# Optimization experiments

Measured on AMD Instinct MI355X. Metric: run time of the kernel, lower is better.

Reference implementation:

```python
import jax, jax.numpy as jnp
import numpy as np

B, C, HW = 32, 512, 4096
NUM_CLASSES = 80


def setup_inputs() -> dict:
    key = jax.random.key(0)
    k1, k2 = jax.random.split(key)
    feats = jax.random.normal(k1, (B, C, HW), dtype=jnp.float32)
    # Conv2d(feat_size, num_classes, 1, bias=False) weight -> [num_classes, feat_size]
    W = jax.random.normal(k2, (NUM_CLASSES, C), dtype=jnp.float32) * (1.0 / np.sqrt(C))
    return {"feats": feats, "W": W}


def reference(feats, W):
    # 1x1 conv == per-pixel matmul: [B,C,HW] x [N,C] -> [B,N,HW]
    att_logits = jnp.einsum('bch,nc->bnh', feats, W)
    att_maps = jax.nn.softmax(att_logits, axis=2)  # softmax over spatial dim HW
    # attention-weighted pooling: [B,N,HW] x [B,HW,C] -> [B,N,C]
    cls_feats = jnp.einsum('bnh,bch->bnc', att_maps, feats)
    return cls_feats
```

## Files before the change

kernel.cpp:

```cpp
#include <hip/hip_runtime.h>

#define B_ 32
#define C_ 512
#define HW_ 4096
#define N_ 80

typedef __bf16 bf16x8 __attribute__((ext_vector_type(8)));
typedef __bf16 bf16x4 __attribute__((ext_vector_type(4)));
typedef float f32x4 __attribute__((ext_vector_type(4)));
typedef unsigned short u16x8 __attribute__((ext_vector_type(8)));

__device__ __forceinline__ void gload_lds16(const void* g, void* l) {
  __builtin_amdgcn_global_load_lds((const __attribute__((address_space(1))) void*)g,
                                   (__attribute__((address_space(3))) void*)l, 16, 0, 0);
}

#define VMCNT(n) asm volatile("s_waitcnt vmcnt(" #n ")" ::: "memory")
#define SBAR() asm volatile("s_barrier" ::: "memory")

__global__ __launch_bounds__(256) void k0_wfrag(const float* __restrict__ W,
                                                __bf16* __restrict__ Wfrag,
                                                float* __restrict__ denom) {
  const int t = blockIdx.x * 256 + threadIdx.x;
  if (t < B_ * N_) denom[t] = 0.f;
  if (t >= 16 * 5 * 64) return;
  const int cs = t / 320, rem = t % 320;
  const int nf = rem >> 6, lane = rem & 63;
  const int n = nf * 16 + (lane & 15);
  const int c = cs * 32 + (lane >> 4) * 8;
  const float* wp = W + (size_t)n * C_ + c;
  bf16x8 v;
#pragma unroll
  for (int i = 0; i < 8; ++i) v[i] = (__bf16)wp[i];
  *(bf16x8*)(Wfrag + (size_t)t * 8) = v;
}

#define K1_STAGE(CS, SLOT)                                                      \
  {                                                                             \
    _Pragma("unroll") for (int j = 0; j < 4; ++j) {                             \
      const int d = j * 256 + tid;                                              \
      const int r = d >> 5, p = d & 31;                                         \
      gload_lds16(fb + (size_t)((CS)*32 + r) * HW_ + htile0 + p * 4,            \
                  (char*)tile + (SLOT)*16384 + (j * 256 + wave * 64) * 16);     \
    }                                                                           \
  }

#define K1_WLOAD(W, CS)                                                         \
  {                                                                             \
    _Pragma("unroll") for (int nf = 0; nf < 5; ++nf)                            \
        W[nf] = *(const u16x8*)(Wfrag + ((size_t)((CS)*5 + nf) * 64 + lane) * 8); \
  }

#define K1_COMPUTE(T, WU)                                                       \
  {                                                                             \
    const float* tb = (const float*)((char*)tile + ((T) % 3) * 16384);          \
    bf16x8 afr[2];                                                              \
    _Pragma("unroll") for (int hf = 0; hf < 2; ++hf) {                          \
      const int col = wave * 32 + hf * 16 + l16;                                \
      _Pragma("unroll") for (int i = 0; i < 8; ++i)                             \
          afr[hf][i] = (__bf16)tb[(quad * 8 + i) * 128 + col];                  \
    }                                                                           \
    _Pragma("unroll") for (int nf = 0; nf < 5; ++nf) {                          \
      const bf16x8 bfr = __builtin_bit_cast(bf16x8, WU[nf]);                    \
      acc[0][nf] = __builtin_amdgcn_mfma_f32_16x16x32_bf16(afr[0], bfr, acc[0][nf], 0, 0, 0); \
      acc[1][nf] = __builtin_amdgcn_mfma_f32_16x16x32_bf16(afr[1], bfr, acc[1][nf], 0, 0, 0); \
    }                                                                           \
  }

#define K1_ITER(T, WU, WL)                                                      \
  {                                                                             \
    VMCNT(9); SBAR();                                                           \
    K1_WLOAD(WL, (T) + 1);                                                      \
    if ((T) + 2 < 16) K1_STAGE((T) + 2, ((T) + 2) % 3);                         \
    K1_COMPUTE(T, WU);                                                          \
  }

__global__ __launch_bounds__(256, 3) void k1_logits(const float* __restrict__ feats,
                                                    const __bf16* __restrict__ Wfrag,
                                                    __bf16* __restrict__ E,
                                                    float* __restrict__ denom) {
  __shared__ float tile[3][32 * 128];
  const int tid = threadIdx.x;
  const int lane = tid & 63, wave = tid >> 6;
  const int quad = lane >> 4, l16 = lane & 15;
  const int b = blockIdx.y;
  const int htile0 = blockIdx.x * 128;
  const float* fb = feats + (size_t)b * (C_ * HW_);

  const f32x4 zero = {0.f, 0.f, 0.f, 0.f};
  f32x4 acc[2][5];
#pragma unroll
  for (int hf = 0; hf < 2; ++hf)
#pragma unroll
    for (int nf = 0; nf < 5; ++nf) acc[hf][nf] = zero;

  u16x8 wfA[5], wfB[5];
  K1_STAGE(0, 0);
  K1_WLOAD(wfA, 0);
  K1_STAGE(1, 1);

  for (int t = 0; t < 14; t += 2) {
    K1_ITER(t, wfA, wfB);
    K1_ITER(t + 1, wfB, wfA);
  }
  K1_ITER(14, wfA, wfB);
  VMCNT(5); SBAR();
  K1_COMPUTE(15, wfB);

#pragma unroll
  for (int nf = 0; nf < 5; ++nf) {
    const int n = nf * 16 + l16;
    float s = 0.f;
#pragma unroll
    for (int hf = 0; hf < 2; ++hf) {
      bf16x4 pk;
#pragma unroll
      for (int j = 0; j < 4; ++j) {
        const float e = __expf(acc[hf][nf][j]);
        s += e;
        pk[j] = (__bf16)e;
      }
      const int h = htile0 + wave * 32 + hf * 16 + quad * 4;
      *(bf16x4*)(E + (size_t)(b * N_ + n) * HW_ + h) = pk;
    }
    s += __shfl_xor(s, 16);
    s += __shfl_xor(s, 32);
    if (lane < 16) atomicAdd(denom + b * N_ + nf * 16 + lane, s);
  }
}

#define K3_STAGE(TK, SLOT)                                                      \
  {                                                                             \
    const int h0 = (TK)*64;                                                     \
    _Pragma("unroll") for (int j = 0; j < 2; ++j) {                             \
      const int d = j * 256 + tid;                                              \
      const int r = d >> 4, p = d & 15;                                         \
      gload_lds16(fb + (size_t)(c0 + r) * HW_ + h0 + ((p ^ (r & 15)) << 2),     \
                  (char*)fA + (SLOT)*8192 + (j * 256 + wave * 64) * 16);        \
    }                                                                           \
    _Pragma("unroll") for (int j = 0; j < 2; ++j) {                             \
      const int d = j * 256 + tid;                                              \
      const int r = d >> 3, p = d & 7;                                          \
      gload_lds16(eb + (size_t)r * HW_ + h0 + ((p ^ (r & 7)) << 3),             \
                  (char*)fB + (SLOT)*10240 + (j * 256 + wave * 64) * 16);       \
    }                                                                           \
    {                                                                           \
      const int d = 512 + (wave & 1) * 64 + lane;                               \
      const int r = d >> 3, p = d & 7;                                          \
      gload_lds16(eb + (size_t)r * HW_ + h0 + ((p ^ (r & 7)) << 3),             \
                  (char*)fB + (SLOT)*10240 + (512 + (wave & 1) * 64) * 16);     \
    }                                                                           \
  }

#define K3_COMPUTE(T)                                                           \
  {                                                                             \
    const float* A = (const float*)((char*)fA + ((T) % 4) * 8192);              \
    const __bf16* Bv = (const __bf16*)((char*)fB + ((T) % 4) * 10240);          \
    _Pragma("unroll") for (int ks = 0; ks < 2; ++ks) {                          \
      const int u0 = (ks * 8 + quad * 2) ^ l16;                                 \
      const int u1 = (ks * 8 + quad * 2 + 1) ^ l16;                             \
      const f32x4 va = *(const f32x4*)&A[rA * 64 + u0 * 4];                     \
      const f32x4 vb = *(const f32x4*)&A[rA * 64 + u1 * 4];                     \
      bf16x8 af;                                                                \
      af[0] = (__bf16)va[0]; af[1] = (__bf16)va[1];                             \
      af[2] = (__bf16)va[2]; af[3] = (__bf16)va[3];                             \
      af[4] = (__bf16)vb[0]; af[5] = (__bf16)vb[1];                             \
      af[6] = (__bf16)vb[2]; af[7] = (__bf16)vb[3];                             \
      _Pragma("unroll") for (int nfl = 0; nfl < 3; ++nfl) {                     \
        if (nfl >= nfcnt) break;                                                \
        const int n = (nfbase + nfl) * 16 + l16;                                \
        const int ub = (ks * 4 + quad) ^ (l16 & 7);                             \
        const u16x8 bv = *(const u16x8*)&Bv[n * 64 + ub * 8];                   \
        const bf16x8 bfr = __builtin_bit_cast(bf16x8, bv);                      \
        acc[nfl] = __builtin_amdgcn_mfma_f32_16x16x32_bf16(af, bfr, acc[nfl], 0, 0, 0); \
      }                                                                         \
    }                                                                           \
  }

__global__ __launch_bounds__(256, 2) void k3_pool(const float* __restrict__ feats,
                                                  const __bf16* __restrict__ E,
                                                  const float* __restrict__ denom,
                                                  float* __restrict__ out) {
  __shared__ float fA[4][32 * 64];
  __shared__ __bf16 fB[4][80 * 64];
  const int tid = threadIdx.x;
  const int lane = tid & 63, wave = tid >> 6;
  const int quad = lane >> 4, l16 = lane & 15;
  const int cf = wave & 1, ng = wave >> 1;
  const int nfbase = ng ? 3 : 0, nfcnt = ng ? 2 : 3;

  const int wg = blockIdx.x;
  const int nid = (wg & 7) * 64 + (wg >> 3);
  const int b = nid >> 4, cx = nid & 15;
  const int c0 = cx * 32;

  const float* fb = feats + (size_t)b * (C_ * HW_);
  const __bf16* eb = E + (size_t)b * N_ * HW_;
  const int rA = cf * 16 + l16;

  const f32x4 zero = {0.f, 0.f, 0.f, 0.f};
  f32x4 acc[3];
#pragma unroll
  for (int i = 0; i < 3; ++i) acc[i] = zero;

  K3_STAGE(0, 0);
  K3_STAGE(1, 1);
  K3_STAGE(2, 2);

  for (int t = 0; t < 61; ++t) {
    VMCNT(10); SBAR();
    K3_STAGE(t + 3, (t + 3) & 3);
    K3_COMPUTE(t);
  }
  VMCNT(10); SBAR(); K3_COMPUTE(61);
  VMCNT(5);  SBAR(); K3_COMPUTE(62);
  VMCNT(0);  SBAR(); K3_COMPUTE(63);

#pragma unroll
  for (int nfl = 0; nfl < 3; ++nfl) {
    if (nfl >= nfcnt) break;
    const int n = (nfbase + nfl) * 16 + l16;
    const float r = 1.0f / denom[b * N_ + n];
    float4 v;
    v.x = acc[nfl][0] * r; v.y = acc[nfl][1] * r;
    v.z = acc[nfl][2] * r; v.w = acc[nfl][3] * r;
    *(float4*)(out + (size_t)(b * N_ + n) * C_ + c0 + cf * 16 + quad * 4) = v;
  }
}

extern "C" void kernel_launch(void* const* d_in, const int* in_sizes, int n_in,
                              void* d_out, int out_size, void* d_ws, size_t ws_size,
                              hipStream_t stream) {
  (void)in_sizes; (void)n_in; (void)out_size; (void)ws_size;
  const float* feats = (const float*)d_in[0];
  const float* Wm = (const float*)d_in[1];
  float* out = (float*)d_out;

  __bf16* E = (__bf16*)d_ws;
  __bf16* Wfrag = E + (size_t)B_ * N_ * HW_;
  float* denom = (float*)(Wfrag + 16 * 5 * 64 * 8);

  hipLaunchKernelGGL(k0_wfrag, dim3(20), dim3(256), 0, stream, Wm, Wfrag, denom);
  hipLaunchKernelGGL(k1_logits, dim3(HW_ / 128, B_), dim3(256), 0, stream, feats, Wfrag, E, denom);
  hipLaunchKernelGGL(k3_pool, dim3(512), dim3(256), 0, stream, feats, E, denom, out);
}
```

Before: 122.3 us.

## Double k3_pool waves to 8 and halve the HW tile per stage

The pooling kernel now runs 512 threads (8 waves) per block instead of 256. The N dimension is split across 4 wave groups (2+1+1+1 fragments), and each pipeline stage covers a 32-wide HW tile instead of 64, which doubles the loop trip count and halves LDS use per stage. Only some lanes issue the global-to-LDS loads, and the wait counts are retuned. The goal is more waves per CU to hide memory latency and better MFMA balance. The cost is twice as many barriers, smaller transfers per stage, and an uneven split of work across waves.

```diff
diff --git a/kernel.cpp b/kernel.cpp
--- a/kernel.cpp
+++ b/kernel.cpp
@@ -131,63 +131,56 @@
 
 #define K3_STAGE(TK, SLOT)                                                      \
   {                                                                             \
-    const int h0 = (TK)*64;                                                     \
-    _Pragma("unroll") for (int j = 0; j < 2; ++j) {                             \
-      const int d = j * 256 + tid;                                              \
-      const int r = d >> 4, p = d & 15;                                         \
-      gload_lds16(fb + (size_t)(c0 + r) * HW_ + h0 + ((p ^ (r & 15)) << 2),     \
-                  (char*)fA + (SLOT)*8192 + (j * 256 + wave * 64) * 16);        \
-    }                                                                           \
-    _Pragma("unroll") for (int j = 0; j < 2; ++j) {                             \
-      const int d = j * 256 + tid;                                              \
+    const int h0 = (TK)*32;                                                     \
+    if (lane < 32) {                                                            \
+      const int d = wave * 32 + lane;                                           \
       const int r = d >> 3, p = d & 7;                                          \
-      gload_lds16(eb + (size_t)r * HW_ + h0 + ((p ^ (r & 7)) << 3),             \
-                  (char*)fB + (SLOT)*10240 + (j * 256 + wave * 64) * 16);       \
-    }                                                                           \
-    {                                                                           \
-      const int d = 512 + (wave & 1) * 64 + lane;                               \
-      const int r = d >> 3, p = d & 7;                                          \
-      gload_lds16(eb + (size_t)r * HW_ + h0 + ((p ^ (r & 7)) << 3),             \
-                  (char*)fB + (SLOT)*10240 + (512 + (wave & 1) * 64) * 16);     \
+      gload_lds16(fb + (size_t)(c0 + r) * HW_ + h0 + ((p ^ (r & 7)) << 2),      \
+                  (char*)fA + (SLOT)*4096 + wave * 512);                        \
+    }                                                                           \
+    if (lane < 40) {                                                            \
+      const int d = wave * 40 + lane;                                           \
+      const int r = d >> 2, p = d & 3;                                          \
+      gload_lds16(eb + (size_t)r * HW_ + h0 + ((p ^ (r & 3)) << 3),             \
+                  (char*)fB + (SLOT)*5120 + wave * 640);                        \
     }                                                                           \
   }
 
 #define K3_COMPUTE(T)                                                           \
   {                                                                             \
-    const float* A = (const float*)((char*)fA + ((T) % 4) * 8192);              \
-    const __bf16* Bv = (const __bf16*)((char*)fB + ((T) % 4) * 10240);          \
-    _Pragma("unroll") for (int ks = 0; ks < 2; ++ks) {                          \
-      const int u0 = (ks * 8 + quad * 2) ^ l16;                                 \
-      const int u1 = (ks * 8 + quad * 2 + 1) ^ l16;                             \
-      const f32x4 va = *(const f32x4*)&A[rA * 64 + u0 * 4];                     \
-      const f32x4 vb = *(const f32x4*)&A[rA * 64 + u1 * 4];                     \
-      bf16x8 af;                                                                \
-      af[0] = (__bf16)va[0]; af[1] = (__bf16)va[1];                             \
-      af[2] = (__bf16)va[2]; af[3] = (__bf16)va[3];                             \
-      af[4] = (__bf16)vb[0]; af[5] = (__bf16)vb[1];                             \
-      af[6] = (__bf16)vb[2]; af[7] = (__bf16)vb[3];                             \
-      _Pragma("unroll") for (int nfl = 0; nfl < 3; ++nfl) {                     \
-        if (nfl >= nfcnt) break;                                                \
-        const int n = (nfbase + nfl) * 16 + l16;                                \
-        const int ub = (ks * 4 + quad) ^ (l16 & 7);                             \
-        const u16x8 bv = *(const u16x8*)&Bv[n * 64 + ub * 8];                   \
-        const bf16x8 bfr = __builtin_bit_cast(bf16x8, bv);                      \
-        acc[nfl] = __builtin_amdgcn_mfma_f32_16x16x32_bf16(af, bfr, acc[nfl], 0, 0, 0); \
-      }                                                                         \
-    }                                                                           \
-  }
-
-__global__ __launch_bounds__(256, 2) void k3_pool(const float* __restrict__ feats,
+    const float* A = (const float*)((char*)fA + ((T) & 3) * 4096);              \
+    const __bf16* Bv = (const __bf16*)((char*)fB + ((T) & 3) * 5120);           \
+    const int u0 = (quad * 2) ^ (l16 & 7);                                      \
+    const int u1 = (quad * 2 + 1) ^ (l16 & 7);                                  \
+    const f32x4 va = *(const f32x4*)&A[rA * 32 + u0 * 4];                       \
+    const f32x4 vb = *(const f32x4*)&A[rA * 32 + u1 * 4];                       \
+    bf16x8 af;                                                                  \
+    af[0] = (__bf16)va[0]; af[1] = (__bf16)va[1];                               \
+    af[2] = (__bf16)va[2]; af[3] = (__bf16)va[3];                               \
+    af[4] = (__bf16)vb[0]; af[5] = (__bf16)vb[1];                               \
+    af[6] = (__bf16)vb[2]; af[7] = (__bf16)vb[3];                               \
+    _Pragma("unroll") for (int nfl = 0; nfl < 2; ++nfl) {                       \
+      if (nfl >= nfcnt) break;                                                  \
+      const int n = (nfbase + nfl) * 16 + l16;                                  \
+      const int ub = quad ^ (l16 & 3);                                          \
+      const u16x8 bv = *(const u16x8*)&Bv[n * 32 + ub * 8];                     \
+      const bf16x8 bfr = __builtin_bit_cast(bf16x8, bv);                        \
+      acc[nfl] = __builtin_amdgcn_mfma_f32_16x16x32_bf16(af, bfr, acc[nfl], 0, 0, 0); \
+    }                                                                           \
+  }
+
+__global__ __launch_bounds__(512, 2) void k3_pool(const float* __restrict__ feats,
                                                   const __bf16* __restrict__ E,
                                                   const float* __restrict__ denom,
                                                   float* __restrict__ out) {
-  __shared__ float fA[4][32 * 64];
-  __shared__ __bf16 fB[4][80 * 64];
+  __shared__ float fA[4 * 32 * 32];
+  __shared__ __bf16 fB[4 * 80 * 32];
   const int tid = threadIdx.x;
   const int lane = tid & 63, wave = tid >> 6;
   const int quad = lane >> 4, l16 = lane & 15;
   const int cf = wave & 1, ng = wave >> 1;
-  const int nfbase = ng ? 3 : 0, nfcnt = ng ? 2 : 3;
+  const int nfbase = (ng == 0) ? 0 : (ng + 1);
+  const int nfcnt = (ng == 0) ? 2 : 1;
 
   const int wg = blockIdx.x;
   const int nid = (wg & 7) * 64 + (wg >> 3);
@@ -197,27 +190,27 @@
   const float* fb = feats + (size_t)b * (C_ * HW_);
   const __bf16* eb = E + (size_t)b * N_ * HW_;
   const int rA = cf * 16 + l16;
-
   const f32x4 zero = {0.f, 0.f, 0.f, 0.f};
-  f32x4 acc[3];
-#pragma unroll
-  for (int i = 0; i < 3; ++i) acc[i] = zero;
+
+  f32x4 acc[2];
+  acc[0] = zero;
+  acc[1] = zero;
 
   K3_STAGE(0, 0);
   K3_STAGE(1, 1);
   K3_STAGE(2, 2);
 
-  for (int t = 0; t < 61; ++t) {
-    VMCNT(10); SBAR();
+  for (int t = 0; t < 125; ++t) {
+    VMCNT(4); SBAR();
     K3_STAGE(t + 3, (t + 3) & 3);
     K3_COMPUTE(t);
   }
-  VMCNT(10); SBAR(); K3_COMPUTE(61);
-  VMCNT(5);  SBAR(); K3_COMPUTE(62);
-  VMCNT(0);  SBAR(); K3_COMPUTE(63);
-
-#pragma unroll
-  for (int nfl = 0; nfl < 3; ++nfl) {
+  VMCNT(4); SBAR(); K3_COMPUTE(125);
+  VMCNT(2); SBAR(); K3_COMPUTE(126);
+  VMCNT(0); SBAR(); K3_COMPUTE(127);
+
+#pragma unroll
+  for (int nfl = 0; nfl < 2; ++nfl) {
     if (nfl >= nfcnt) break;
     const int n = (nfbase + nfl) * 16 + l16;
     const float r = 1.0f / denom[b * N_ + n];
@@ -242,5 +235,5 @@
 
   hipLaunchKernelGGL(k0_wfrag, dim3(20), dim3(256), 0, stream, Wm, Wfrag, denom);
   hipLaunchKernelGGL(k1_logits, dim3(HW_ / 128, B_), dim3(256), 0, stream, feats, Wfrag, E, denom);
-  hipLaunchKernelGGL(k3_pool, dim3(512), dim3(256), 0, stream, feats, E, denom, out);
-}
+  hipLaunchKernelGGL(k3_pool, dim3(512), dim3(512), 0, stream, feats, E, denom, out);
+}
```

Measured after the change: 154.2 us. 1.26x slower.

## Load attention fragments directly into registers and widen feats LDS tiles

Applied to the files above, without the earlier changes.

The pooling kernel stops staging the bf16 exp-logit matrix E through LDS. Each wave now loads its B-operand fragments straight from global memory into double-buffered registers, one step ahead of use. The feats tile is widened to 128 spatial positions per stage, and the loop is restructured with adjusted vmcnt waits and the min-blocks launch bound removed. This is meant to cut LDS traffic and barrier overhead, at the cost of more VGPRs, lower occupancy and less coalesced global reads of E.

```diff
diff --git a/kernel.cpp b/kernel.cpp
--- a/kernel.cpp
+++ b/kernel.cpp
@@ -129,60 +129,61 @@
   }
 }
 
-#define K3_STAGE(TK, SLOT)                                                      \
-  {                                                                             \
-    const int h0 = (TK)*64;                                                     \
-    _Pragma("unroll") for (int j = 0; j < 2; ++j) {                             \
+#define K3_STAGE(T, SLOT)                                                       \
+  {                                                                             \
+    _Pragma("unroll") for (int j = 0; j < 4; ++j) {                             \
       const int d = j * 256 + tid;                                              \
-      const int r = d >> 4, p = d & 15;                                         \
-      gload_lds16(fb + (size_t)(c0 + r) * HW_ + h0 + ((p ^ (r & 15)) << 2),     \
-                  (char*)fA + (SLOT)*8192 + (j * 256 + wave * 64) * 16);        \
-    }                                                                           \
-    _Pragma("unroll") for (int j = 0; j < 2; ++j) {                             \
-      const int d = j * 256 + tid;                                              \
-      const int r = d >> 3, p = d & 7;                                          \
-      gload_lds16(eb + (size_t)r * HW_ + h0 + ((p ^ (r & 7)) << 3),             \
-                  (char*)fB + (SLOT)*10240 + (j * 256 + wave * 64) * 16);       \
-    }                                                                           \
-    {                                                                           \
-      const int d = 512 + (wave & 1) * 64 + lane;                               \
-      const int r = d >> 3, p = d & 7;                                          \
-      gload_lds16(eb + (size_t)r * HW_ + h0 + ((p ^ (r & 7)) << 3),             \
-                  (char*)fB + (SLOT)*10240 + (512 + (wave & 1) * 64) * 16);     \
-    }                                                                           \
-  }
-
-#define K3_COMPUTE(T)                                                           \
-  {                                                                             \
-    const float* A = (const float*)((char*)fA + ((T) % 4) * 8192);              \
-    const __bf16* Bv = (const __bf16*)((char*)fB + ((T) % 4) * 10240);          \
-    _Pragma("unroll") for (int ks = 0; ks < 2; ++ks) {                          \
-      const int u0 = (ks * 8 + quad * 2) ^ l16;                                 \
-      const int u1 = (ks * 8 + quad * 2 + 1) ^ l16;                             \
-      const f32x4 va = *(const f32x4*)&A[rA * 64 + u0 * 4];                     \
-      const f32x4 vb = *(const f32x4*)&A[rA * 64 + u1 * 4];                     \
+      const int r = d >> 5, p = d & 31;                                         \
+      gload_lds16(fb + (size_t)(c0 + r) * HW_ + (T)*128 + ((p ^ (r & 15)) << 2), \
+                  (char*)fA + (SLOT)*16384 + (j * 256 + wave * 64) * 16);       \
+    }                                                                           \
+  }
+
+#define K3_BFRAG(DST, T)                                                        \
+  {                                                                             \
+    _Pragma("unroll") for (int ks_ = 0; ks_ < 4; ++ks_)                         \
+    _Pragma("unroll") for (int nf_ = 0; nf_ < 3; ++nf_)                         \
+      if (nf_ < nfcnt) {                                                        \
+        const int n_ = (nfbase + nf_) * 16 + l16;                               \
+        DST[ks_][nf_] =                                                         \
+            *(const u16x8*)(eb + (size_t)n_ * HW_ + (T)*128 + ks_ * 32 + quad * 8); \
+      }                                                                         \
+  }
+
+#define K3_COMPUTE(T, BFS)                                                      \
+  {                                                                             \
+    const float* A = (const float*)((char*)fA + ((T)&3) * 16384);               \
+    _Pragma("unroll") for (int ks_ = 0; ks_ < 4; ++ks_) {                       \
+      const int u0 = (ks_ * 8 + quad * 2) ^ (rA & 15);                          \
+      const int u1 = (ks_ * 8 + quad * 2 + 1) ^ (rA & 15);                      \
+      const f32x4 va = *(const f32x4*)&A[rA * 128 + u0 * 4];                    \
+      const f32x4 vb = *(const f32x4*)&A[rA * 128 + u1 * 4];                    \
       bf16x8 af;                                                                \
       af[0] = (__bf16)va[0]; af[1] = (__bf16)va[1];                             \
       af[2] = (__bf16)va[2]; af[3] = (__bf16)va[3];                             \
       af[4] = (__bf16)vb[0]; af[5] = (__bf16)vb[1];                             \
       af[6] = (__bf16)vb[2]; af[7] = (__bf16)vb[3];                             \
-      _Pragma("unroll") for (int nfl = 0; nfl < 3; ++nfl) {                     \
-        if (nfl >= nfcnt) break;                                                \
-        const int n = (nfbase + nfl) * 16 + l16;                                \
-        const int ub = (ks * 4 + quad) ^ (l16 & 7);                             \
-        const u16x8 bv = *(const u16x8*)&Bv[n * 64 + ub * 8];                   \
-        const bf16x8 bfr = __builtin_bit_cast(bf16x8, bv);                      \
-        acc[nfl] = __builtin_amdgcn_mfma_f32_16x16x32_bf16(af, bfr, acc[nfl], 0, 0, 0); \
-      }                                                                         \
-    }                                                                           \
-  }
-
-__global__ __launch_bounds__(256, 2) void k3_pool(const float* __restrict__ feats,
-                                                  const __bf16* __restrict__ E,
-                                                  const float* __restrict__ denom,
-                                                  float* __restrict__ out) {
-  __shared__ float fA[4][32 * 64];
-  __shared__ __bf16 fB[4][80 * 64];
+      _Pragma("unroll") for (int nf_ = 0; nf_ < 3; ++nf_)                       \
+        if (nf_ < nfcnt) {                                                      \
+          const bf16x8 bfr = __builtin_bit_cast(bf16x8, BFS[ks_][nf_]);         \
+          acc[nf_] = __builtin_amdgcn_mfma_f32_16x16x32_bf16(af, bfr, acc[nf_], 0, 0, 0); \
+        }                                                                       \
+    }                                                                           \
+  }
+
+#define K3_ITER(T, USE, LOADDST)                                                \
+  {                                                                             \
+    VMCNT(4); SBAR();                                                           \
+    K3_BFRAG(LOADDST, (T) + 1);                                                 \
+    K3_STAGE((T) + 3, ((T) + 3) & 3);                                           \
+    K3_COMPUTE(T, USE);                                                         \
+  }
+
+__global__ __launch_bounds__(256) void k3_pool(const float* __restrict__ feats,
+                                               const __bf16* __restrict__ E,
+                                               const float* __restrict__ denom,
+                                               float* __restrict__ out) {
+  __shared__ float fA[4 * 32 * 128];
   const int tid = threadIdx.x;
   const int lane = tid & 63, wave = tid >> 6;
   const int quad = lane >> 4, l16 = lane & 15;
@@ -197,24 +198,35 @@
   const float* fb = feats + (size_t)b * (C_ * HW_);
   const __bf16* eb = E + (size_t)b * N_ * HW_;
   const int rA = cf * 16 + l16;
-
   const f32x4 zero = {0.f, 0.f, 0.f, 0.f};
+
   f32x4 acc[3];
 #pragma unroll
   for (int i = 0; i < 3; ++i) acc[i] = zero;
 
+  u16x8 bfA[4][3], bfB[4][3];
+  K3_BFRAG(bfA, 0);
   K3_STAGE(0, 0);
   K3_STAGE(1, 1);
   K3_STAGE(2, 2);
 
-  for (int t = 0; t < 61; ++t) {
-    VMCNT(10); SBAR();
-    K3_STAGE(t + 3, (t + 3) & 3);
-    K3_COMPUTE(t);
-  }
-  VMCNT(10); SBAR(); K3_COMPUTE(61);
-  VMCNT(5);  SBAR(); K3_COMPUTE(62);
-  VMCNT(0);  SBAR(); K3_COMPUTE(63);
+  VMCNT(8); SBAR();
+  K3_BFRAG(bfB, 1);
+  K3_STAGE(3, 3);
+  K3_COMPUTE(0, bfA);
+
+  for (int t = 1; t < 28; t += 2) {
+    K3_ITER(t, bfB, bfA);
+    K3_ITER(t + 1, bfA, bfB);
+  }
+  VMCNT(4); SBAR();
+  K3_BFRAG(bfA, 30);
+  K3_COMPUTE(29, bfB);
+  VMCNT(0); SBAR();
+  K3_BFRAG(bfB, 31);
+  K3_COMPUTE(30, bfA);
+  VMCNT(0); SBAR();
+  K3_COMPUTE(31, bfB);
 
 #pragma unroll
   for (int nfl = 0; nfl < 3; ++nfl) {
```

Result: slower. 151.4 us (+23.8%).
